# Performance work log

Hardware: AMD Instinct MI355X
Metric: run time of the kernel (lower is better)

Reference implementation:

```python
import jax, jax.numpy as jnp
import numpy as np

N_ATOMS = 25000
IN_FEATURES = 128
OUT_FEATURES = 128
N_SPECIES = 64


def setup_inputs() -> dict:
    key = jax.random.key(0)
    k1, k2, k3, k4 = jax.random.split(key, 4)
    features = jax.random.normal(k1, (N_ATOMS, IN_FEATURES), dtype=jnp.float32)
    species_idx = jax.random.randint(k2, (N_ATOMS,), 0, N_SPECIES, dtype=jnp.int64)
    # kaiming_uniform_ with a=sqrt(5) on fan_in gives bound = 1/sqrt(fan_in);
    # bias init uses the same bound.
    bound = 1.0 / np.sqrt(IN_FEATURES)
    weight = jax.random.uniform(
        k3, (N_SPECIES, OUT_FEATURES, IN_FEATURES), dtype=jnp.float32,
        minval=-bound, maxval=bound)
    bias = jax.random.uniform(
        k4, (N_SPECIES, OUT_FEATURES), dtype=jnp.float32,
        minval=-bound, maxval=bound)
    return {"features": features, "species_idx": species_idx,
            "weight": weight, "bias": bias}


def reference(features, species_idx, weight, bias):
    # Species-indexed weight gather + per-atom GEMV (batched matmul with q=1).
    # W[idx]: (n_atoms, out_features, in_features)
    W = jnp.take(weight, species_idx, axis=0)
    b = jnp.take(bias, species_idx, axis=0)  # (n_atoms, out_features)
    out = jnp.einsum("ni,noi->no", features, W) + b
    return out
```

## Files before the change

kernel.cpp:

```cpp
#include <hip/hip_runtime.h>

#define NATOMS 25000
#define NSP 64
#define NRANGE 8
#define RSIZE ((NATOMS + NRANGE - 1) / NRANGE)
#define WSUB ((RSIZE + 3) / 4)
#define WIT ((WSUB + 63) / 64)
#define LCAP (WIT * 64)

typedef short bf16x8 __attribute__((ext_vector_type(8)));
typedef float f32x4  __attribute__((ext_vector_type(4)));
typedef unsigned short u16;

__device__ __forceinline__ u16 f2bf(float f) {
  unsigned u = __float_as_uint(f);
  u += 0x7fffu + ((u >> 16) & 1u);
  return (u16)(u >> 16);
}

__global__ __launch_bounds__(256)
void zcl_kernel(const float* __restrict__ feat,
                const int*   __restrict__ sp,
                const float* __restrict__ weight,
                const float* __restrict__ bias,
                float*       __restrict__ out)
{
  __shared__ u16 Ws[128 * 128];
  __shared__ u16 wlist[4][LCAP];

  const int tid = threadIdx.x;
  const int bid = blockIdx.x;
  const int s  = bid >> 3;
  const int r  = bid & 7;
  const int lo = r * RSIZE;
  const int hi = (lo + RSIZE < NATOMS) ? (lo + RSIZE) : NATOMS;

  const int wv   = tid >> 6;
  const int lane = tid & 63;
  const int l16  = lane & 15;
  const int kq   = lane >> 4;
  const int wlo  = lo + wv * WSUB;
  const int whi  = (wlo + WSUB < hi) ? (wlo + WSUB) : hi;

  int spv[WIT];
  #pragma unroll
  for (int i = 0; i < WIT; ++i) {
    int a = wlo + i * 64 + lane;
    spv[i] = (a < whi) ? sp[a] : -1;
  }

  float bvb[8];
  #pragma unroll
  for (int nf = 0; nf < 8; ++nf) bvb[nf] = bias[s * 128 + l16 + 16 * nf];

  const float4* wg = (const float4*)(weight + (size_t)s * (128 * 128));
  float4 w0[8], w1[8];
  #pragma unroll
  for (int j = 0; j < 8; ++j) {
    int m = j * 256 + tid;
    int row = m >> 4, c = m & 15;
    w0[j] = wg[row * 32 + c * 2];
    w1[j] = wg[row * 32 + c * 2 + 1];
  }

  int wcnt = 0;
  #pragma unroll
  for (int i = 0; i < WIT; ++i) {
    bool m = (spv[i] == s);
    unsigned long long mk = __ballot(m);
    if (m) wlist[wv][wcnt + __popcll(mk & ((1ull << lane) - 1ull))] =
             (u16)(wlo + i * 64 + lane);
    wcnt += (int)__popcll(mk);
  }
  const int nt = (wcnt + 15) >> 4;

  float4 pf[8];
  if (nt > 0) {
    int li = l16;
    int atomA = wlist[wv][li < wcnt ? li : 0];
    const float4* xg = (const float4*)(feat + (size_t)atomA * 128);
    #pragma unroll
    for (int ks = 0; ks < 4; ++ks) {
      pf[2 * ks]     = xg[ks * 8 + kq * 2];
      pf[2 * ks + 1] = xg[ks * 8 + kq * 2 + 1];
    }
  }

  #pragma unroll
  for (int j = 0; j < 8; ++j) {
    int m = j * 256 + tid;
    int row = m >> 4, c = m & 15;
    union { u16 h[8]; bf16x8 v; } uu;
    uu.h[0] = f2bf(w0[j].x); uu.h[1] = f2bf(w0[j].y);
    uu.h[2] = f2bf(w0[j].z); uu.h[3] = f2bf(w0[j].w);
    uu.h[4] = f2bf(w1[j].x); uu.h[5] = f2bf(w1[j].y);
    uu.h[6] = f2bf(w1[j].z); uu.h[7] = f2bf(w1[j].w);
    *(bf16x8*)&Ws[row * 128 + ((c ^ (row & 7)) << 3)] = uu.v;
  }

  __syncthreads();

  for (int t = 0; t < nt; ++t) {
    bf16x8 av[4];
    #pragma unroll
    for (int ks = 0; ks < 4; ++ks) {
      union { u16 h[8]; bf16x8 v; } uu;
      uu.h[0] = f2bf(pf[2 * ks].x);     uu.h[1] = f2bf(pf[2 * ks].y);
      uu.h[2] = f2bf(pf[2 * ks].z);     uu.h[3] = f2bf(pf[2 * ks].w);
      uu.h[4] = f2bf(pf[2 * ks + 1].x); uu.h[5] = f2bf(pf[2 * ks + 1].y);
      uu.h[6] = f2bf(pf[2 * ks + 1].z); uu.h[7] = f2bf(pf[2 * ks + 1].w);
      av[ks] = uu.v;
    }

    if (t + 1 < nt) {
      int li = (t + 1) * 16 + l16;
      int atomA = wlist[wv][li < wcnt ? li : 0];
      const float4* xg = (const float4*)(feat + (size_t)atomA * 128);
      #pragma unroll
      for (int ks = 0; ks < 4; ++ks) {
        pf[2 * ks]     = xg[ks * 8 + kq * 2];
        pf[2 * ks + 1] = xg[ks * 8 + kq * 2 + 1];
      }
    }

    f32x4 acc[8];
    #pragma unroll
    for (int nf = 0; nf < 8; ++nf) acc[nf] = (f32x4){0.f, 0.f, 0.f, 0.f};
    #pragma unroll
    for (int ks = 0; ks < 4; ++ks) {
      int chunk = ((ks * 4 + kq) ^ (l16 & 7)) << 3;
      #pragma unroll
      for (int nf = 0; nf < 8; ++nf) {
        bf16x8 b = *(const bf16x8*)&Ws[(l16 + 16 * nf) * 128 + chunk];
        acc[nf] = __builtin_amdgcn_mfma_f32_16x16x32_bf16(av[ks], b, acc[nf], 0, 0, 0);
      }
    }

    #pragma unroll
    for (int q = 0; q < 4; ++q) {
      int li2 = t * 16 + kq * 4 + q;
      if (li2 < wcnt) {
        int atom = wlist[wv][li2];
        float* op = out + (size_t)atom * 128 + l16;
        #pragma unroll
        for (int nf = 0; nf < 8; ++nf) op[16 * nf] = acc[nf][q] + bvb[nf];
      }
    }
  }
}

extern "C" void kernel_launch(void* const* d_in, const int* in_sizes, int n_in,
                              void* d_out, int out_size, void* d_ws, size_t ws_size,
                              hipStream_t stream) {
  const float* feat   = (const float*)d_in[0];
  const int*   sp     = (const int*)d_in[1];
  const float* weight = (const float*)d_in[2];
  const float* bias   = (const float*)d_in[3];
  float*       out    = (float*)d_out;
  zcl_kernel<<<NSP * NRANGE, 256, 0, stream>>>(feat, sp, weight, bias, out);
}
```

Baseline: 17.35 us.

## Split into prep kernel building per-species atom lists and bf16 weights

Adds a prep kernel that converts all weights to bf16 in the workspace and builds per-species atom lists with shared- and global-memory atomics. The main kernel then loads the pre-converted weights straight into LDS with global_load_lds, reads its atoms from the precomputed list, and maps blocks to XCDs by species. This removes the per-block scan of every species index and the repeated fp32 weight conversion. In exchange it adds a memset, a second kernel launch and workspace traffic. It also assumes at most 1024 atoms per species and that 8 blocks of 4 waves (512 atoms) cover each species; any atoms beyond that are never computed.

```diff
diff --git a/kernel.cpp b/kernel.cpp
--- a/kernel.cpp
+++ b/kernel.cpp
@@ -2,15 +2,14 @@
 
 #define NATOMS 25000
 #define NSP 64
-#define NRANGE 8
-#define RSIZE ((NATOMS + NRANGE - 1) / NRANGE)
-#define WSUB ((RSIZE + 3) / 4)
-#define WIT ((WSUB + 63) / 64)
-#define LCAP (WIT * 64)
+#define LISTCAP 1024
+#define NBLK_A ((NATOMS + 255) / 256)
 
 typedef short bf16x8 __attribute__((ext_vector_type(8)));
 typedef float f32x4  __attribute__((ext_vector_type(4)));
 typedef unsigned short u16;
+typedef __attribute__((address_space(3))) unsigned int lds_u32;
+typedef __attribute__((address_space(1))) unsigned int gbl_u32;
 
 __device__ __forceinline__ u16 f2bf(float f) {
   unsigned u = __float_as_uint(f);
@@ -18,67 +17,77 @@
   return (u16)(u >> 16);
 }
 
+
 __global__ __launch_bounds__(256)
-void zcl_kernel(const float* __restrict__ feat,
-                const int*   __restrict__ sp,
-                const float* __restrict__ weight,
-                const float* __restrict__ bias,
-                float*       __restrict__ out)
+void prep_kernel(const float* __restrict__ w, const int* __restrict__ sp,
+                 u16* __restrict__ wbf, int* __restrict__ cnt, int* __restrict__ lists)
+{
+  __shared__ int lh[NSP];
+  __shared__ int lbase[NSP];
+  const int tid = threadIdx.x, bid = blockIdx.x;
+  const int g = bid * 256 + tid;
+
+  const float4* p = (const float4*)w + (size_t)g * 2;
+  float4 v0 = p[0], v1 = p[1];
+  union { u16 h[8]; bf16x8 v; } uu;
+  uu.h[0] = f2bf(v0.x); uu.h[1] = f2bf(v0.y);
+  uu.h[2] = f2bf(v0.z); uu.h[3] = f2bf(v0.w);
+  uu.h[4] = f2bf(v1.x); uu.h[5] = f2bf(v1.y);
+  uu.h[6] = f2bf(v1.z); uu.h[7] = f2bf(v1.w);
+  ((bf16x8*)wbf)[g] = uu.v;
+
+  if (bid < NBLK_A) {
+    if (tid < NSP) lh[tid] = 0;
+    __syncthreads();
+    int a = g, s = 0, lpos = 0;
+    bool valid = (a < NATOMS);
+    if (valid) { s = sp[a]; lpos = atomicAdd(&lh[s], 1); }
+    __syncthreads();
+    if (tid < NSP) lbase[tid] = atomicAdd(&cnt[tid], lh[tid]);
+    __syncthreads();
+    if (valid) lists[s * LISTCAP + lbase[s] + lpos] = a;
+  }
+}
+
+__global__ __launch_bounds__(256)
+void zcl_main(const float* __restrict__ feat, const u16* __restrict__ wbf,
+              const float* __restrict__ bias, const int* __restrict__ cnt,
+              const int* __restrict__ lists, float* __restrict__ out)
 {
   __shared__ u16 Ws[128 * 128];
-  __shared__ u16 wlist[4][LCAP];
 
-  const int tid = threadIdx.x;
-  const int bid = blockIdx.x;
-  const int s  = bid >> 3;
-  const int r  = bid & 7;
-  const int lo = r * RSIZE;
-  const int hi = (lo + RSIZE < NATOMS) ? (lo + RSIZE) : NATOMS;
+  const int tid = threadIdx.x, bid = blockIdx.x;
+  const int xcd = bid & 7, qq = bid >> 3;
+  const int s = xcd + 8 * (qq & 7);
+  const int j = qq >> 3;
+  const int wv = tid >> 6, lane = tid & 63;
+  const int l16 = lane & 15, kq = lane >> 4;
 
-  const int wv   = tid >> 6;
-  const int lane = tid & 63;
-  const int l16  = lane & 15;
-  const int kq   = lane >> 4;
-  const int wlo  = lo + wv * WSUB;
-  const int whi  = (wlo + WSUB < hi) ? (wlo + WSUB) : hi;
-
-  int spv[WIT];
+  const u16* wsrc = wbf + (size_t)s * 16384;
   #pragma unroll
-  for (int i = 0; i < WIT; ++i) {
-    int a = wlo + i * 64 + lane;
-    spv[i] = (a < whi) ? sp[a] : -1;
+  for (int rnd = 0; rnd < 8; ++rnd) {
+    int m = rnd * 256 + tid, row = m >> 4, c = m & 15;
+    const u16* src = wsrc + row * 128 + ((c ^ (row & 7)) << 3);
+    u16* dst = &Ws[(rnd * 256 + (tid & ~63)) * 8];
+    __builtin_amdgcn_global_load_lds((gbl_u32*)src, (lds_u32*)dst, 16, 0, 0);
   }
 
+  const int cntS = cnt[s];
+  const int t  = j + 8 * wv;
+  const int li = t * 16 + l16;
+  const int specA = lists[s * LISTCAP + li];
+  const int d0    = lists[s * LISTCAP];
   float bvb[8];
   #pragma unroll
   for (int nf = 0; nf < 8; ++nf) bvb[nf] = bias[s * 128 + l16 + 16 * nf];
 
-  const float4* wg = (const float4*)(weight + (size_t)s * (128 * 128));
-  float4 w0[8], w1[8];
-  #pragma unroll
-  for (int j = 0; j < 8; ++j) {
-    int m = j * 256 + tid;
-    int row = m >> 4, c = m & 15;
-    w0[j] = wg[row * 32 + c * 2];
-    w1[j] = wg[row * 32 + c * 2 + 1];
-  }
+  if (cntS == 0) return;
+  const bool run = (t * 16 < cntS);
 
-  int wcnt = 0;
-  #pragma unroll
-  for (int i = 0; i < WIT; ++i) {
-    bool m = (spv[i] == s);
-    unsigned long long mk = __ballot(m);
-    if (m) wlist[wv][wcnt + __popcll(mk & ((1ull << lane) - 1ull))] =
-             (u16)(wlo + i * 64 + lane);
-    wcnt += (int)__popcll(mk);
-  }
-  const int nt = (wcnt + 15) >> 4;
-
+  int a0 = (li < cntS) ? specA : d0;
   float4 pf[8];
-  if (nt > 0) {
-    int li = l16;
-    int atomA = wlist[wv][li < wcnt ? li : 0];
-    const float4* xg = (const float4*)(feat + (size_t)atomA * 128);
+  if (run) {
+    const float4* xg = (const float4*)(feat + (size_t)a0 * 128);
     #pragma unroll
     for (int ks = 0; ks < 4; ++ks) {
       pf[2 * ks]     = xg[ks * 8 + kq * 2];
@@ -86,65 +95,41 @@
     }
   }
 
+  __syncthreads();
+  if (!run) return;
+
+  bf16x8 av[4];
   #pragma unroll
-  for (int j = 0; j < 8; ++j) {
-    int m = j * 256 + tid;
-    int row = m >> 4, c = m & 15;
+  for (int ks = 0; ks < 4; ++ks) {
     union { u16 h[8]; bf16x8 v; } uu;
-    uu.h[0] = f2bf(w0[j].x); uu.h[1] = f2bf(w0[j].y);
-    uu.h[2] = f2bf(w0[j].z); uu.h[3] = f2bf(w0[j].w);
-    uu.h[4] = f2bf(w1[j].x); uu.h[5] = f2bf(w1[j].y);
-    uu.h[6] = f2bf(w1[j].z); uu.h[7] = f2bf(w1[j].w);
-    *(bf16x8*)&Ws[row * 128 + ((c ^ (row & 7)) << 3)] = uu.v;
+    uu.h[0] = f2bf(pf[2 * ks].x);     uu.h[1] = f2bf(pf[2 * ks].y);
+    uu.h[2] = f2bf(pf[2 * ks].z);     uu.h[3] = f2bf(pf[2 * ks].w);
+    uu.h[4] = f2bf(pf[2 * ks + 1].x); uu.h[5] = f2bf(pf[2 * ks + 1].y);
+    uu.h[6] = f2bf(pf[2 * ks + 1].z); uu.h[7] = f2bf(pf[2 * ks + 1].w);
+    av[ks] = uu.v;
   }
 
-  __syncthreads();
+  f32x4 acc[8];
+  #pragma unroll
+  for (int nf = 0; nf < 8; ++nf) acc[nf] = (f32x4){0.f, 0.f, 0.f, 0.f};
+  #pragma unroll
+  for (int ks = 0; ks < 4; ++ks) {
+    int chunk = ((ks * 4 + kq) ^ (l16 & 7)) << 3;
+    #pragma unroll
+    for (int nf = 0; nf < 8; ++nf) {
+      bf16x8 b = *(const bf16x8*)&Ws[(l16 + 16 * nf) * 128 + chunk];
+      acc[nf] = __builtin_amdgcn_mfma_f32_16x16x32_bf16(av[ks], b, acc[nf], 0, 0, 0);
+    }
+  }
 
-  for (int t = 0; t < nt; ++t) {
-    bf16x8 av[4];
-    #pragma unroll
-    for (int ks = 0; ks < 4; ++ks) {
-      union { u16 h[8]; bf16x8 v; } uu;
-      uu.h[0] = f2bf(pf[2 * ks].x);     uu.h[1] = f2bf(pf[2 * ks].y);
-      uu.h[2] = f2bf(pf[2 * ks].z);     uu.h[3] = f2bf(pf[2 * ks].w);
-      uu.h[4] = f2bf(pf[2 * ks + 1].x); uu.h[5] = f2bf(pf[2 * ks + 1].y);
-      uu.h[6] = f2bf(pf[2 * ks + 1].z); uu.h[7] = f2bf(pf[2 * ks + 1].w);
-      av[ks] = uu.v;
-    }
-
-    if (t + 1 < nt) {
-      int li = (t + 1) * 16 + l16;
-      int atomA = wlist[wv][li < wcnt ? li : 0];
-      const float4* xg = (const float4*)(feat + (size_t)atomA * 128);
+  #pragma unroll
+  for (int qr = 0; qr < 4; ++qr) {
+    int rr = kq * 4 + qr;
+    int a_row = __shfl(a0, rr);
+    if (t * 16 + rr < cntS) {
+      float* op = out + (size_t)a_row * 128 + l16;
       #pragma unroll
-      for (int ks = 0; ks < 4; ++ks) {
-        pf[2 * ks]     = xg[ks * 8 + kq * 2];
-        pf[2 * ks + 1] = xg[ks * 8 + kq * 2 + 1];
-      }
-    }
-
-    f32x4 acc[8];
-    #pragma unroll
-    for (int nf = 0; nf < 8; ++nf) acc[nf] = (f32x4){0.f, 0.f, 0.f, 0.f};
-    #pragma unroll
-    for (int ks = 0; ks < 4; ++ks) {
-      int chunk = ((ks * 4 + kq) ^ (l16 & 7)) << 3;
-      #pragma unroll
-      for (int nf = 0; nf < 8; ++nf) {
-        bf16x8 b = *(const bf16x8*)&Ws[(l16 + 16 * nf) * 128 + chunk];
-        acc[nf] = __builtin_amdgcn_mfma_f32_16x16x32_bf16(av[ks], b, acc[nf], 0, 0, 0);
-      }
-    }
-
-    #pragma unroll
-    for (int q = 0; q < 4; ++q) {
-      int li2 = t * 16 + kq * 4 + q;
-      if (li2 < wcnt) {
-        int atom = wlist[wv][li2];
-        float* op = out + (size_t)atom * 128 + l16;
-        #pragma unroll
-        for (int nf = 0; nf < 8; ++nf) op[16 * nf] = acc[nf][q] + bvb[nf];
-      }
+      for (int nf = 0; nf < 8; ++nf) op[16 * nf] = acc[nf][qr] + bvb[nf];
     }
   }
 }
@@ -157,5 +142,13 @@
   const float* weight = (const float*)d_in[2];
   const float* bias   = (const float*)d_in[3];
   float*       out    = (float*)d_out;
-  zcl_kernel<<<NSP * NRANGE, 256, 0, stream>>>(feat, sp, weight, bias, out);
+
+  char* base = (char*)d_ws;
+  u16*  wbf   = (u16*)base;
+  int*  cnt   = (int*)(base + (2u << 20));
+  int*  lists = (int*)(base + (2u << 20) + 4096);
+
+  hipMemsetAsync(cnt, 0, NSP * sizeof(int), stream);
+  prep_kernel<<<512, 256, 0, stream>>>(weight, sp, wbf, cnt, lists);
+  zcl_main<<<NSP * 8, 256, 0, stream>>>(feat, wbf, bias, cnt, lists, out);
 }
```

Measured after the change: 20.57 us. +18.6%, slower.
